# Kernel optimization log

Measured on AMD Instinct MI355X. Metric: run time of the kernel, lower is better.

## Reference

```python
import jax, jax.numpy as jnp
import numpy as np

B, N, HIST, D, E, NH = 1024, 2, 64, 256, 128, 8
HD = D // NH


def _linear_params(key, fan_in, fan_out):
    kw, kb = jax.random.split(key)
    lim = 1.0 / np.sqrt(fan_in)
    W = jax.random.uniform(kw, (fan_in, fan_out), jnp.float32, -lim, lim)
    b = jax.random.uniform(kb, (fan_out,), jnp.float32, -lim, lim)
    return W, b


def setup_inputs() -> dict:
    key = jax.random.key(0)
    ks = jax.random.split(key, 11)
    inp = {
        "node_features": jax.random.normal(ks[0], (B, N, HIST, D), jnp.float32),
        "edge_features": jax.random.normal(ks[1], (B, E), jnp.float32),
    }
    inp["Wq"], inp["bq"] = _linear_params(ks[2], D, D)
    inp["Wk"], inp["bk"] = _linear_params(ks[3], D, D)
    inp["Wv"], inp["bv"] = _linear_params(ks[4], D, D)
    inp["Wo"], inp["bo"] = _linear_params(ks[5], D, D)
    inp["Wbias"], inp["bbias"] = _linear_params(ks[6], E, NH)
    inp["Wgate"], inp["bgate"] = _linear_params(ks[7], E, D)
    inp["Wscale"], inp["bscale"] = _linear_params(ks[8], E, D)
    inp["Wshift"], inp["bshift"] = _linear_params(ks[9], E, D)
    inp["Whead"], inp["bhead"] = _linear_params(ks[10], E, NH)
    return inp


def reference(node_features, edge_features, Wq, bq, Wk, bk, Wv, bv, Wo, bo,
              Wbias, bbias, Wgate, bgate, Wscale, bscale, Wshift, bshift,
              Whead, bhead) -> jnp.ndarray:
    b, n, hist, d = node_features.shape
    s = n * hist  # seq_len (temporal mode)
    x = node_features.reshape(b, s, d)

    Q = x @ Wq + bq
    K = x @ Wk + bk
    V = x @ Wv + bv

    # Edge-conditioned modulation of V (ECC-style gate/scale/shift)
    gate = jax.nn.sigmoid(edge_features @ Wgate + bgate)      # [b, d]
    scale = jnp.tanh(edge_features @ Wscale + bscale)         # [b, d]
    shift = edge_features @ Wshift + bshift                   # [b, d]
    V = (V * (1.0 + scale[:, None, :]) + shift[:, None, :]) * gate[:, None, :]

    # [b, nh, s, hd]
    Q = Q.reshape(b, s, NH, HD).transpose(0, 2, 1, 3)
    K = K.reshape(b, s, NH, HD).transpose(0, 2, 1, 3)
    V = V.reshape(b, s, NH, HD).transpose(0, 2, 1, 3)

    scores = jnp.einsum('bhqd,bhkd->bhqk', Q, K) * (1.0 / np.sqrt(HD))

    edge_bias = edge_features @ Wbias + bbias                 # [b, nh]
    head_scale = jnp.tanh(edge_features @ Whead + bhead)      # [b, nh]
    scores = scores * (1.0 + head_scale[:, :, None, None])

    # attention bias: edge_bias placed at (t, hist+t) and (hist+t, t)
    t = jnp.arange(hist)
    eb = jnp.broadcast_to(edge_bias[:, :, None], (b, NH, hist))
    attention_bias = jnp.zeros((b, NH, s, s), scores.dtype)
    attention_bias = attention_bias.at[:, :, t, hist + t].set(eb)
    attention_bias = attention_bias.at[:, :, hist + t, t].set(eb)

    attn = jax.nn.softmax(scores + attention_bias, axis=-1)   # dropout in eval mode = identity
    out = jnp.einsum('bhqk,bhkd->bhqd', attn, V)
    out = out.transpose(0, 2, 1, 3).reshape(b, n, hist, d)
    out = out[:, :, -1, :]                                    # last timestep per node
    return out @ Wo + bo
```

## Files before the change

### kernel.cpp

```cpp
#include <hip/hip_runtime.h>
#include <cstdint>
#include <cstddef>


typedef short bf16x8 __attribute__((ext_vector_type(8)));
typedef float f32x4 __attribute__((ext_vector_type(4)));

#define MFMA16(A, B, C) __builtin_amdgcn_mfma_f32_16x16x32_bf16((A), (B), (C), 0, 0, 0)

static __device__ __forceinline__ uint16_t f2bf(float f) {
    uint32_t u = __builtin_bit_cast(uint32_t, f);
    u += 0x7FFFu + ((u >> 16) & 1u);
    return (uint16_t)(u >> 16);
}
static __device__ __forceinline__ uint32_t pack2(float a, float b) {
    return (uint32_t)f2bf(a) | ((uint32_t)f2bf(b) << 16);
}

__global__ __launch_bounds__(256) void k_wt(
    const float* __restrict__ Wq, const float* __restrict__ Wv,
    const float* __restrict__ Wo, const float* __restrict__ Wk,
    uint16_t* __restrict__ WqT, uint16_t* __restrict__ WvT,
    uint16_t* __restrict__ WoT, uint16_t* __restrict__ WkB)
{
    const int t = threadIdx.x;
    const int tr = blockIdx.x, tc = blockIdx.y, z = blockIdx.z;
    if (z == 3) {
        #pragma unroll
        for (int i = 0; i < 16; i++) {
            int flat = i * 256 + t;
            int lr = flat >> 6, lc = flat & 63;
            WkB[(size_t)(tr * 64 + lr) * 264 + tc * 64 + lc] =
                f2bf(Wk[(size_t)(tr * 64 + lr) * 256 + tc * 64 + lc]);
        }
        return;
    }
    const float* W = (z == 0) ? Wq : ((z == 1) ? Wv : Wo);
    uint16_t* O = (z == 0) ? WqT : ((z == 1) ? WvT : WoT);
    __shared__ float tile[64][65];
    #pragma unroll
    for (int i = 0; i < 16; i++) {
        int flat = i * 256 + t;
        int lr = flat >> 6, lc = flat & 63;
        tile[lr][lc] = W[(size_t)(tr * 64 + lr) * 256 + tc * 64 + lc];
    }
    __syncthreads();
    #pragma unroll
    for (int i = 0; i < 16; i++) {
        int flat = i * 256 + t;
        int orow = flat >> 6, oc = flat & 63;
        O[(size_t)(tc * 64 + orow) * 264 + tr * 64 + oc] = f2bf(tile[oc][orow]);
    }
}

__global__ __launch_bounds__(256) void k_eq(
    const float* __restrict__ edge,
    const float* __restrict__ Wgate, const float* __restrict__ bgate,
    const float* __restrict__ Wscale, const float* __restrict__ bscale,
    const float* __restrict__ Wshift, const float* __restrict__ bshift,
    const float* __restrict__ Wbias, const float* __restrict__ bbias,
    const float* __restrict__ Whead, const float* __restrict__ bhead,
    float* __restrict__ sp, float* __restrict__ tp, float* __restrict__ ebhs,
    const float* __restrict__ node, const uint16_t* __restrict__ WqT,
    const uint16_t* __restrict__ WkB, const float* __restrict__ bq,
    uint16_t* __restrict__ U)
{
    __shared__ char smem[2 * 16 * 264 * 2];
    const int t = threadIdx.x;
    if (blockIdx.x < 256) {
        float* eL = (float*)smem;
        const int b0 = blockIdx.x * 4;
        for (int idx = t; idx < 512; idx += 256) {
            int bi = idx >> 7, e = idx & 127;
            eL[bi * 128 + e] = edge[(size_t)(b0 + bi) * 128 + e];
        }
        __syncthreads();
        float ag[4] = {0, 0, 0, 0}, asr[4] = {0, 0, 0, 0}, ah[4] = {0, 0, 0, 0};
        for (int e = 0; e < 128; e++) {
            float wg = Wgate[e * 256 + t];
            float wsc = Wscale[e * 256 + t];
            float wsh = Wshift[e * 256 + t];
            #pragma unroll
            for (int bi = 0; bi < 4; bi++) {
                float xv = eL[bi * 128 + e];
                ag[bi] = fmaf(xv, wg, ag[bi]);
                asr[bi] = fmaf(xv, wsc, asr[bi]);
                ah[bi] = fmaf(xv, wsh, ah[bi]);
            }
        }
        float bg = bgate[t], bs = bscale[t], bsh = bshift[t];
        #pragma unroll
        for (int bi = 0; bi < 4; bi++) {
            float g = 1.0f / (1.0f + __expf(-(ag[bi] + bg)));
            float sc = tanhf(asr[bi] + bs);
            float sh = ah[bi] + bsh;
            sp[(size_t)(b0 + bi) * 256 + t] = (1.0f + sc) * g;
            tp[(size_t)(b0 + bi) * 256 + t] = sh * g;
        }
        if (t < 64) {
            int bi = t >> 4, o = t & 15, h = o & 7;
            const float* W = (o < 8) ? Wbias : Whead;
            float a = 0.0f;
            for (int e = 0; e < 128; e++) a = fmaf(eL[bi * 128 + e], W[e * 8 + h], a);
            float val = (o < 8) ? (a + bbias[h]) : tanhf(a + bhead[h]);
            ebhs[(size_t)(b0 + bi) * 16 + o] = val;
        }
        return;
    }
    uint16_t* xq = (uint16_t*)smem;
    uint16_t* QL = (uint16_t*)smem + 16 * 264;
    const int lane = t & 63, w = t >> 6, c = lane & 15, quad = lane >> 4;
    const int b0 = (blockIdx.x - 256) * 4;
    #pragma unroll
    for (int i = 0; i < 4; i++) {
        int flat4 = i * 256 + t;
        int row = flat4 >> 6, c4 = flat4 & 63;
        int r = row & 7;
        int bb = b0 + (r >> 1);
        int s = (r & 1) ? 127 : 63;
        const float4 v = *(const float4*)(node + ((size_t)(bb * 128 + s)) * 256 + c4 * 4);
        uint2 pv; pv.x = pack2(v.x, v.y); pv.y = pack2(v.z, v.w);
        *(uint2*)&xq[row * 264 + c4 * 4] = pv;
    }
    __syncthreads();
    f32x4 zero = {0, 0, 0, 0};
    f32x4 acc[4];
    #pragma unroll
    for (int i = 0; i < 4; i++) acc[i] = zero;
    #pragma unroll
    for (int kk = 0; kk < 8; kk++) {
        bf16x8 afr = *(const bf16x8*)&xq[c * 264 + kk * 32 + quad * 8];
        #pragma unroll
        for (int i = 0; i < 4; i++) {
            int nt = w * 4 + i;
            bf16x8 bfr = *(const bf16x8*)&WqT[(size_t)(nt * 16 + c) * 264 + kk * 32 + quad * 8];
            acc[i] = MFMA16(afr, bfr, acc[i]);
        }
    }
    #pragma unroll
    for (int i = 0; i < 4; i++) {
        int nt = w * 4 + i;
        float bqv = bq[nt * 16 + c];
        #pragma unroll
        for (int r = 0; r < 4; r++) {
            QL[(quad * 4 + r) * 264 + nt * 16 + c] = f2bf(acc[i][r] + bqv);
        }
    }
    __syncthreads();
    for (int hh = 0; hh < 8; hh++) {
        bf16x8 bfr = *(const bf16x8*)&QL[c * 264 + hh * 32 + quad * 8];
        #pragma unroll
        for (int i = 0; i < 4; i++) {
            int mt = w * 4 + i;
            bf16x8 afr = *(const bf16x8*)&WkB[(size_t)(mt * 16 + c) * 264 + hh * 32 + quad * 8];
            f32x4 d = MFMA16(afr, bfr, zero);
            if (c < 8) {
                int bb = b0 + (c >> 1);
                int qh = (c & 1) * 8 + hh;
                uint2 pk; pk.x = pack2(d[0], d[1]); pk.y = pack2(d[2], d[3]);
                *(uint2*)&U[((size_t)(bb * 16 + qh)) * 256 + mt * 16 + quad * 4] = pk;
            }
        }
    }
}

__global__ __launch_bounds__(256, 2) void k_mo(
    const float* __restrict__ node,
    const uint16_t* __restrict__ U,
    const float* __restrict__ ebhs,
    const uint16_t* __restrict__ WvT, const uint16_t* __restrict__ WoT,
    const float* __restrict__ bv, const float* __restrict__ bo,
    const float* __restrict__ sp, const float* __restrict__ tp,
    float* __restrict__ out)
{
    __shared__ uint16_t xc[64 * 264];
    __shared__ uint16_t uL[64 * 264];
    __shared__ uint16_t pL[4 * 16 * 72];
    __shared__ float ebhsL[64];
    const int b0 = blockIdx.x * 4;
    const int t = threadIdx.x, lane = t & 63, w = t >> 6, c = lane & 15, quad = lane >> 4;

    #pragma unroll
    for (int i = 0; i < 8; i++) {
        int id = i * 256 + t;
        int row = id >> 5, c16 = id & 31;
        uint4 v = *(const uint4*)&U[((size_t)(b0 * 16) + row) * 256 + c16 * 8];
        *(uint4*)&uL[row * 264 + c16 * 8] = v;
    }
    if (t < 64) ebhsL[t] = ebhs[(size_t)b0 * 16 + t];

    float4 R[16];
    #pragma unroll
    for (int i = 0; i < 16; i++) {
        int f4 = i * 256 + t;
        int row = f4 >> 6, c4 = f4 & 63;
        R[i] = *(const float4*)(node + ((size_t)(b0)*128 + row) * 256 + c4 * 4);
    }
    #pragma unroll
    for (int i = 0; i < 16; i++) {
        int f4 = i * 256 + t;
        int row = f4 >> 6, c4 = f4 & 63;
        uint2 pv; pv.x = pack2(R[i].x, R[i].y); pv.y = pack2(R[i].z, R[i].w);
        int col = (c4 * 4 + ((row >> 3) & 3) * 16) & 255;
        *(uint2*)&xc[row * 264 + col] = pv;
    }
    __syncthreads();

    const int q = c >> 3, h = c & 7;
    f32x4 zero = {0, 0, 0, 0};
    f32x4 yacc[4][4];
    #pragma unroll
    for (int bi = 0; bi < 4; bi++)
        #pragma unroll
        for (int tt = 0; tt < 4; tt++) yacc[bi][tt] = zero;
    float mrow[4] = {-1e30f, -1e30f, -1e30f, -1e30f};
    float lrow[4] = {0, 0, 0, 0};
    uint16_t* pW = &pL[w * 16 * 72];

    for (int p = 0; p < 8; p++) {
        const int bi = p >> 1, ch = p & 1;
        if (p < 7) {
            int nbi = (p + 1) >> 1, nch = (p + 1) & 1;
            #pragma unroll
            for (int i = 0; i < 16; i++) {
                int f4 = i * 256 + t;
                int row = f4 >> 6, c4 = f4 & 63;
                R[i] = *(const float4*)(node + ((size_t)(b0 + nbi) * 128 + nch * 64 + row) * 256 + c4 * 4);
            }
        }
        const float scaleF = 0.17677669529663687f * (1.0f + ebhsL[bi * 16 + 8 + h]);
        const float ebv = ebhsL[bi * 16 + h];
        f32x4 sacc[4];
        #pragma unroll
        for (int kt = 0; kt < 4; kt++) sacc[kt] = zero;
        #pragma unroll
        for (int kk = 0; kk < 8; kk++) {
            bf16x8 bfr = *(const bf16x8*)&uL[(bi * 16 + c) * 264 + kk * 32 + quad * 8];
            #pragma unroll
            for (int kt = 0; kt < 4; kt++) {
                int arow = kt * 16 + c;
                int sh = ((arow >> 3) & 3) * 16;
                int colA = (kk * 32 + quad * 8 + sh) & 255;
                bf16x8 afr = *(const bf16x8*)&xc[arow * 264 + colA];
                sacc[kt] = MFMA16(afr, bfr, sacc[kt]);
            }
        }
        float v0[4][4];
        float lmax = -1e30f;
        #pragma unroll
        for (int kt = 0; kt < 4; kt++) {
            #pragma unroll
            for (int r = 0; r < 4; r++) {
                int krow = ch * 64 + kt * 16 + quad * 4 + r;
                float x = sacc[kt][r] * scaleF;
                if ((q == 0 && krow == 127) || (q == 1 && krow == 63)) x += ebv;
                v0[kt][r] = x;
                lmax = fmaxf(lmax, x);
            }
        }
        lmax = fmaxf(lmax, __shfl_xor(lmax, 16, 64));
        lmax = fmaxf(lmax, __shfl_xor(lmax, 32, 64));
        float mnew = fmaxf(mrow[bi], lmax);
        float alpha = __expf(mrow[bi] - mnew);
        float lsum = 0.0f;
        #pragma unroll
        for (int kt = 0; kt < 4; kt++) {
            float p0 = __expf(v0[kt][0] - mnew);
            float p1 = __expf(v0[kt][1] - mnew);
            float p2 = __expf(v0[kt][2] - mnew);
            float p3 = __expf(v0[kt][3] - mnew);
            lsum += (p0 + p1) + (p2 + p3);
            uint2 pk; pk.x = pack2(p0, p1); pk.y = pack2(p2, p3);
            *(uint2*)&pW[c * 72 + kt * 16 + quad * 4] = pk;
        }
        lsum += __shfl_xor(lsum, 16, 64);
        lsum += __shfl_xor(lsum, 32, 64);
        lrow[bi] = lrow[bi] * alpha + lsum;
        mrow[bi] = mnew;
        #pragma unroll
        for (int r = 0; r < 4; r++) {
            float aj = __shfl(alpha, quad * 4 + r, 64);
            #pragma unroll
            for (int tt = 0; tt < 4; tt++) yacc[bi][tt][r] *= aj;
        }
        #pragma unroll
        for (int kk = 0; kk < 2; kk++) {
            bf16x8 afr = *(const bf16x8*)&pW[c * 72 + kk * 32 + quad * 8];
            int kbase = kk * 32 + quad * 8;
            int sh = ((kbase >> 3) & 3) * 16;
            #pragma unroll
            for (int tt = 0; tt < 4; tt++) {
                int n = w * 64 + tt * 16 + c;
                int col = (n + sh) & 255;
                union { bf16x8 v; uint32_t u[4]; } bb;
                #pragma unroll
                for (int jj = 0; jj < 4; jj++) {
                    uint32_t lo = xc[(kbase + 2 * jj) * 264 + col];
                    uint32_t hi = xc[(kbase + 2 * jj + 1) * 264 + col];
                    bb.u[jj] = lo | (hi << 16);
                }
                yacc[bi][tt] = MFMA16(afr, bb.v, yacc[bi][tt]);
            }
        }
        if (p < 7) {
            __syncthreads();
            #pragma unroll
            for (int i = 0; i < 16; i++) {
                int f4 = i * 256 + t;
                int row = f4 >> 6, c4 = f4 & 63;
                uint2 pv; pv.x = pack2(R[i].x, R[i].y); pv.y = pack2(R[i].z, R[i].w);
                int col = (c4 * 4 + ((row >> 3) & 3) * 16) & 255;
                *(uint2*)&xc[row * 264 + col] = pv;
            }
            __syncthreads();
        }
    }

    __syncthreads();
    uint16_t* yL = uL;
    #pragma unroll
    for (int bi = 0; bi < 4; bi++) {
        float invr = 1.0f / lrow[bi];
        #pragma unroll
        for (int r = 0; r < 4; r++) {
            float invj = __shfl(invr, quad * 4 + r, 64);
            #pragma unroll
            for (int tt = 0; tt < 4; tt++) {
                int n = w * 64 + tt * 16 + c;
                yL[(bi * 16 + quad * 4 + r) * 264 + n] = f2bf(yacc[bi][tt][r] * invj);
            }
        }
    }
    __syncthreads();
    uint16_t* zm = xc;
    #pragma unroll
    for (int hi = 0; hi < 2; hi++) {
        int hh = w * 2 + hi;
        f32x4 zacc[2];
        zacc[0] = zero; zacc[1] = zero;
        int mr = c & 7;
        int yrow = (mr >> 1) * 16 + (mr & 1) * 8 + hh;
        #pragma unroll
        for (int kk = 0; kk < 8; kk++) {
            bf16x8 afr = *(const bf16x8*)&yL[yrow * 264 + kk * 32 + quad * 8];
            #pragma unroll
            for (int nt = 0; nt < 2; nt++) {
                bf16x8 bfr = *(const bf16x8*)&WvT[(size_t)(hh * 32 + nt * 16 + c) * 264 + kk * 32 + quad * 8];
                zacc[nt] = MFMA16(afr, bfr, zacc[nt]);
            }
        }
        #pragma unroll
        for (int nt = 0; nt < 2; nt++) {
            int col = hh * 32 + nt * 16 + c;
            float bvv = bv[col];
            #pragma unroll
            for (int r = 0; r < 4; r++) {
                int m = quad * 4 + r;
                if (m < 8) {
                    int bb = b0 + (m >> 1);
                    float z = zacc[nt][r] + bvv;
                    zm[m * 264 + col] = f2bf(z * sp[(size_t)bb * 256 + col] + tp[(size_t)bb * 256 + col]);
                }
            }
        }
    }
    __syncthreads();
    #pragma unroll
    for (int i = 0; i < 4; i++) {
        int n = (w * 4 + i) * 16 + c;
        f32x4 fa = zero;
        #pragma unroll
        for (int kk = 0; kk < 8; kk++) {
            bf16x8 afr = *(const bf16x8*)&zm[(c & 7) * 264 + kk * 32 + quad * 8];
            bf16x8 bfr = *(const bf16x8*)&WoT[(size_t)n * 264 + kk * 32 + quad * 8];
            fa = MFMA16(afr, bfr, fa);
        }
        float bov = bo[n];
        #pragma unroll
        for (int r = 0; r < 4; r++) {
            int m = quad * 4 + r;
            if (m < 8) out[(size_t)(b0 * 2 + m) * 256 + n] = fa[r] + bov;
        }
    }
}

extern "C" void kernel_launch(void* const* d_in, const int* in_sizes, int n_in,
                              void* d_out, int out_size, void* d_ws, size_t ws_size,
                              hipStream_t stream) {
    const float* node   = (const float*)d_in[0];
    const float* edge   = (const float*)d_in[1];
    const float* Wq     = (const float*)d_in[2];
    const float* bq     = (const float*)d_in[3];
    const float* Wk     = (const float*)d_in[4];
    const float* Wv     = (const float*)d_in[6];
    const float* bv     = (const float*)d_in[7];
    const float* Wo     = (const float*)d_in[8];
    const float* bo     = (const float*)d_in[9];
    const float* Wbias  = (const float*)d_in[10];
    const float* bbias  = (const float*)d_in[11];
    const float* Wgate  = (const float*)d_in[12];
    const float* bgate  = (const float*)d_in[13];
    const float* Wscale = (const float*)d_in[14];
    const float* bscale = (const float*)d_in[15];
    const float* Wshift = (const float*)d_in[16];
    const float* bshift = (const float*)d_in[17];
    const float* Whead  = (const float*)d_in[18];
    const float* bhead  = (const float*)d_in[19];

    char* ws = (char*)d_ws;
    uint16_t* WqT  = (uint16_t*)(ws + 0);
    uint16_t* WvT  = (uint16_t*)(ws + 135168);
    uint16_t* WoT  = (uint16_t*)(ws + 270336);
    uint16_t* WkB  = (uint16_t*)(ws + 405504);
    float*    spw  = (float*)(ws + 540672);
    float*    tpw  = (float*)(ws + 1589248);
    float*    ebhs = (float*)(ws + 2637824);
    uint16_t* Uw   = (uint16_t*)(ws + 2703360);

    k_wt<<<dim3(4, 4, 4), 256, 0, stream>>>(Wq, Wv, Wo, Wk, WqT, WvT, WoT, WkB);
    k_eq<<<512, 256, 0, stream>>>(edge, Wgate, bgate, Wscale, bscale, Wshift, bshift,
                                  Wbias, bbias, Whead, bhead, spw, tpw, ebhs,
                                  node, WqT, WkB, bq, Uw);
    k_mo<<<256, 256, 0, stream>>>(node, Uw, ebhs, WvT, WoT, bv, bo, spw, tpw,
                                  (float*)d_out);
}
```

Measured before the change: 309.1 us.

## Process one batch per block in k_mo to raise grid size and occupancy

The main attention kernel now gives each block one batch element instead of four, so the grid grows from 256 to 1024 blocks. Shared memory for U and the per-batch edge terms shrinks, the per-batch accumulator arrays become scalars, and launch bounds are raised to three blocks per CU. The aim is to fill all CUs and hide memory latency with more resident blocks. In exchange, each block no longer prefetches the next batch's node data across iterations, and the Wv/Wo projection MFMAs now run with only 2 useful rows out of 16, so weight reads are repeated four times more often.

```diff
diff --git a/kernel.cpp b/kernel.cpp
--- a/kernel.cpp
+++ b/kernel.cpp
@@ -164,7 +164,7 @@
     }
 }
 
-__global__ __launch_bounds__(256, 2) void k_mo(
+__global__ __launch_bounds__(256, 3) void k_mo(
     const float* __restrict__ node,
     const uint16_t* __restrict__ U,
     const float* __restrict__ ebhs,
@@ -174,27 +174,27 @@
     float* __restrict__ out)
 {
     __shared__ uint16_t xc[64 * 264];
-    __shared__ uint16_t uL[64 * 264];
+    __shared__ uint16_t uL[16 * 264];
     __shared__ uint16_t pL[4 * 16 * 72];
-    __shared__ float ebhsL[64];
-    const int b0 = blockIdx.x * 4;
+    __shared__ float ebhsL[16];
+    const int b = blockIdx.x;
     const int t = threadIdx.x, lane = t & 63, w = t >> 6, c = lane & 15, quad = lane >> 4;
 
     #pragma unroll
-    for (int i = 0; i < 8; i++) {
-        int id = i * 256 + t;
-        int row = id >> 5, c16 = id & 31;
-        uint4 v = *(const uint4*)&U[((size_t)(b0 * 16) + row) * 256 + c16 * 8];
+    for (int i = 0; i < 2; i++) {
+        int flat = i * 256 + t;
+        int row = flat >> 5, c16 = flat & 31;
+        uint4 v = *(const uint4*)&U[((size_t)b * 16 + row) * 256 + c16 * 8];
         *(uint4*)&uL[row * 264 + c16 * 8] = v;
     }
-    if (t < 64) ebhsL[t] = ebhs[(size_t)b0 * 16 + t];
+    if (t < 16) ebhsL[t] = ebhs[(size_t)b * 16 + t];
 
     float4 R[16];
     #pragma unroll
     for (int i = 0; i < 16; i++) {
         int f4 = i * 256 + t;
         int row = f4 >> 6, c4 = f4 & 63;
-        R[i] = *(const float4*)(node + ((size_t)(b0)*128 + row) * 256 + c4 * 4);
+        R[i] = *(const float4*)(node + ((size_t)b * 128 + row) * 256 + c4 * 4);
     }
     #pragma unroll
     for (int i = 0; i < 16; i++) {
@@ -207,35 +207,31 @@
     __syncthreads();
 
     const int q = c >> 3, h = c & 7;
+    const float scaleF = 0.17677669529663687f * (1.0f + ebhsL[8 + h]);
+    const float ebv = ebhsL[h];
     f32x4 zero = {0, 0, 0, 0};
-    f32x4 yacc[4][4];
-    #pragma unroll
-    for (int bi = 0; bi < 4; bi++)
-        #pragma unroll
-        for (int tt = 0; tt < 4; tt++) yacc[bi][tt] = zero;
-    float mrow[4] = {-1e30f, -1e30f, -1e30f, -1e30f};
-    float lrow[4] = {0, 0, 0, 0};
+    f32x4 yacc[4];
+    #pragma unroll
+    for (int tt = 0; tt < 4; tt++) yacc[tt] = zero;
+    float mrow = -1e30f, lrow = 0.0f;
     uint16_t* pW = &pL[w * 16 * 72];
 
-    for (int p = 0; p < 8; p++) {
-        const int bi = p >> 1, ch = p & 1;
-        if (p < 7) {
-            int nbi = (p + 1) >> 1, nch = (p + 1) & 1;
+    #pragma unroll
+    for (int ch = 0; ch < 2; ch++) {
+        if (ch == 0) {
             #pragma unroll
             for (int i = 0; i < 16; i++) {
                 int f4 = i * 256 + t;
                 int row = f4 >> 6, c4 = f4 & 63;
-                R[i] = *(const float4*)(node + ((size_t)(b0 + nbi) * 128 + nch * 64 + row) * 256 + c4 * 4);
-            }
-        }
-        const float scaleF = 0.17677669529663687f * (1.0f + ebhsL[bi * 16 + 8 + h]);
-        const float ebv = ebhsL[bi * 16 + h];
+                R[i] = *(const float4*)(node + ((size_t)b * 128 + 64 + row) * 256 + c4 * 4);
+            }
+        }
         f32x4 sacc[4];
         #pragma unroll
         for (int kt = 0; kt < 4; kt++) sacc[kt] = zero;
         #pragma unroll
         for (int kk = 0; kk < 8; kk++) {
-            bf16x8 bfr = *(const bf16x8*)&uL[(bi * 16 + c) * 264 + kk * 32 + quad * 8];
+            bf16x8 bfr = *(const bf16x8*)&uL[c * 264 + kk * 32 + quad * 8];
             #pragma unroll
             for (int kt = 0; kt < 4; kt++) {
                 int arow = kt * 16 + c;
@@ -260,8 +256,8 @@
         }
         lmax = fmaxf(lmax, __shfl_xor(lmax, 16, 64));
         lmax = fmaxf(lmax, __shfl_xor(lmax, 32, 64));
-        float mnew = fmaxf(mrow[bi], lmax);
-        float alpha = __expf(mrow[bi] - mnew);
+        float mnew = fmaxf(mrow, lmax);
+        float alpha = __expf(mrow - mnew);
         float lsum = 0.0f;
         #pragma unroll
         for (int kt = 0; kt < 4; kt++) {
@@ -275,13 +271,13 @@
         }
         lsum += __shfl_xor(lsum, 16, 64);
         lsum += __shfl_xor(lsum, 32, 64);
-        lrow[bi] = lrow[bi] * alpha + lsum;
-        mrow[bi] = mnew;
+        lrow = lrow * alpha + lsum;
+        mrow = mnew;
         #pragma unroll
         for (int r = 0; r < 4; r++) {
             float aj = __shfl(alpha, quad * 4 + r, 64);
             #pragma unroll
-            for (int tt = 0; tt < 4; tt++) yacc[bi][tt][r] *= aj;
+            for (int tt = 0; tt < 4; tt++) yacc[tt][r] *= aj;
         }
         #pragma unroll
         for (int kk = 0; kk < 2; kk++) {
@@ -299,10 +295,10 @@
                     uint32_t hi = xc[(kbase + 2 * jj + 1) * 264 + col];
                     bb.u[jj] = lo | (hi << 16);
                 }
-                yacc[bi][tt] = MFMA16(afr, bb.v, yacc[bi][tt]);
-            }
-        }
-        if (p < 7) {
+                yacc[tt] = MFMA16(afr, bb.v, yacc[tt]);
+            }
+        }
+        if (ch == 0) {
             __syncthreads();
             #pragma unroll
             for (int i = 0; i < 16; i++) {
@@ -318,16 +314,15 @@
 
     __syncthreads();
     uint16_t* yL = uL;
-    #pragma unroll
-    for (int bi = 0; bi < 4; bi++) {
-        float invr = 1.0f / lrow[bi];
+    {
+        float invr = 1.0f / lrow;
         #pragma unroll
         for (int r = 0; r < 4; r++) {
             float invj = __shfl(invr, quad * 4 + r, 64);
             #pragma unroll
             for (int tt = 0; tt < 4; tt++) {
                 int n = w * 64 + tt * 16 + c;
-                yL[(bi * 16 + quad * 4 + r) * 264 + n] = f2bf(yacc[bi][tt][r] * invj);
+                yL[(quad * 4 + r) * 264 + n] = f2bf(yacc[tt][r] * invj);
             }
         }
     }
@@ -338,8 +333,7 @@
         int hh = w * 2 + hi;
         f32x4 zacc[2];
         zacc[0] = zero; zacc[1] = zero;
-        int mr = c & 7;
-        int yrow = (mr >> 1) * 16 + (mr & 1) * 8 + hh;
+        int yrow = (c & 1) * 8 + hh;
         #pragma unroll
         for (int kk = 0; kk < 8; kk++) {
             bf16x8 afr = *(const bf16x8*)&yL[yrow * 264 + kk * 32 + quad * 8];
@@ -356,10 +350,9 @@
             #pragma unroll
             for (int r = 0; r < 4; r++) {
                 int m = quad * 4 + r;
-                if (m < 8) {
-                    int bb = b0 + (m >> 1);
+                if (m < 2) {
                     float z = zacc[nt][r] + bvv;
-                    zm[m * 264 + col] = f2bf(z * sp[(size_t)bb * 256 + col] + tp[(size_t)bb * 256 + col]);
+                    zm[m * 264 + col] = f2bf(z * sp[(size_t)b * 256 + col] + tp[(size_t)b * 256 + col]);
                 }
             }
         }
@@ -371,7 +364,7 @@
         f32x4 fa = zero;
         #pragma unroll
         for (int kk = 0; kk < 8; kk++) {
-            bf16x8 afr = *(const bf16x8*)&zm[(c & 7) * 264 + kk * 32 + quad * 8];
+            bf16x8 afr = *(const bf16x8*)&zm[(c & 1) * 264 + kk * 32 + quad * 8];
             bf16x8 bfr = *(const bf16x8*)&WoT[(size_t)n * 264 + kk * 32 + quad * 8];
             fa = MFMA16(afr, bfr, fa);
         }
@@ -379,7 +372,7 @@
         #pragma unroll
         for (int r = 0; r < 4; r++) {
             int m = quad * 4 + r;
-            if (m < 8) out[(size_t)(b0 * 2 + m) * 256 + n] = fa[r] + bov;
+            if (m < 2) out[(size_t)(b * 2 + m) * 256 + n] = fa[r] + bov;
         }
     }
 }
@@ -421,6 +414,6 @@
     k_eq<<<512, 256, 0, stream>>>(edge, Wgate, bgate, Wscale, bscale, Wshift, bshift,
                                   Wbias, bbias, Whead, bhead, spw, tpw, ebhs,
                                   node, WqT, WkB, bq, Uw);
-    k_mo<<<256, 256, 0, stream>>>(node, Uw, ebhs, WvT, WoT, bv, bo, spw, tpw,
-                                  (float*)d_out);
-}
+    k_mo<<<1024, 256, 0, stream>>>(node, Uw, ebhs, WvT, WoT, bv, bo, spw, tpw,
+                                   (float*)d_out);
+}
```

New measurement: 279.5 us. 1.11x faster.
